# Kernel tuning notes

Hardware: AMD Instinct MI355X
Metric: run time of the kernel (lower is better)

The kernel has to match this reference:

```python
import jax, jax.numpy as jnp
import numpy as np

N_MOD = 2      # len(l_matrix)
N_SUB = 4096   # each l_matrix entry
DIM = 64
K = 20
ALPHA = 3.0
N = N_MOD * N_SUB  # 8192 total nodes


def setup_inputs() -> dict:
    key = jax.random.key(0)
    k1, k2, k3, k4 = jax.random.split(key, 4)
    nmat = N_MOD * N_MOD
    emb1 = 0.1 * jax.random.normal(k1, (nmat, N_SUB, DIM), dtype=jnp.float32)
    emb2 = 0.1 * jax.random.normal(k2, (nmat, N_SUB, DIM), dtype=jnp.float32)
    # __init__ sets w1/w2 to identity, b to zeros; perturb slightly so they matter
    eye = jnp.eye(DIM, dtype=jnp.float32)
    w1 = eye[None] + 0.01 * jax.random.normal(k3, (nmat, DIM, DIM), dtype=jnp.float32)
    w2 = eye[None] + 0.01 * jax.random.normal(k4, (nmat, DIM, DIM), dtype=jnp.float32)
    b1 = jnp.zeros((nmat, DIM), dtype=jnp.float32)
    b2 = jnp.zeros((nmat, DIM), dtype=jnp.float32)
    idx = jnp.arange(N, dtype=jnp.int64) if jax.config.jax_enable_x64 else jnp.arange(N, dtype=jnp.int32)
    return {"idx": idx, "emb1": emb1, "emb2": emb2, "w1": w1, "w2": w2, "b1": b1, "b2": b2}


def reference(idx, emb1, emb2, w1, w2, b1, b2):
    # per-block linear: nodevec = emb @ w + b   (batched over the nmatrix blocks)
    v1 = jnp.einsum('knd,kde->kne', emb1, w1) + b1[:, None, :]   # [nmat, N_SUB, DIM]
    v2 = jnp.einsum('kmd,kde->kme', emb2, w2) + b2[:, None, :]
    # per-block score: relu(tanh(alpha * v1 @ v2^T))
    a = jnp.einsum('kne,kme->knm', v1, v2)                       # [nmat, N_SUB, N_SUB]
    blocks = jax.nn.relu(jnp.tanh(ALPHA * a))
    # assemble full adjacency: block (i,j) at index i*n_mod + j
    adj = blocks.reshape(N_MOD, N_MOD, N_SUB, N_SUB)
    adj = adj.transpose(0, 2, 1, 3).reshape(N, N)                # [N, N]
    # row-wise topk mask (mask=1 at topk positions), adj * mask
    vals, cols = jax.lax.top_k(adj, K)                           # [N, K]
    rows = jnp.arange(N)[:, None]
    out = jnp.zeros_like(adj).at[rows, cols].set(vals)
    return out


if __name__ == "__main__":
    out = reference(**setup_inputs())
    print(out.shape, float(out.sum()))
```

## Files before the change

### kernel.cpp

```cpp
#include <hip/hip_runtime.h>
#include <hip/hip_bf16.h>

#define NSUB 4096
#define DIM 64
#define NROW 8192
#define KTOP 20
#define CAND 64

typedef unsigned long long u64;
typedef __attribute__((ext_vector_type(8))) short bf16x8;
typedef __attribute__((ext_vector_type(4))) float f32x4;

__device__ __forceinline__ unsigned umax(unsigned a, unsigned b) { return a > b ? a : b; }
__device__ __forceinline__ unsigned umin(unsigned a, unsigned b) { return a < b ? a : b; }

__global__ __launch_bounds__(256) void k_compute_v(
        const float* __restrict__ emb1, const float* __restrict__ w1,
        const float* __restrict__ b1,
        const float* __restrict__ emb2, const float* __restrict__ w2,
        const float* __restrict__ b2,
        double* __restrict__ V1d, double* __restrict__ V2d,
        unsigned short* __restrict__ V1b, unsigned short* __restrict__ V2b) {
    __shared__ alignas(16) float embS[64 * 64];
    __shared__ alignas(16) float wS[64 * 64];
    __shared__ float bS[64];

    int bx    = blockIdx.x;
    int which = bx >> 8;
    int rem   = bx & 255;
    int k     = rem >> 6;
    int tile  = rem & 63;
    int n0    = tile * 64;

    const float* emb = which ? emb2 : emb1;
    const float* w   = which ? w2 : w1;
    const float* b   = which ? b2 : b1;
    double* Vd = which ? V2d : V1d;
    unsigned short* Vb = which ? V2b : V1b;

    int tid = threadIdx.x;
    const float* esrc = emb + ((size_t)k * NSUB + n0) * DIM;
    const float* wsrc = w + (size_t)k * DIM * DIM;
    for (int t = tid; t < 64 * 64; t += 256) { embS[t] = esrc[t]; wS[t] = wsrc[t]; }
    if (tid < 64) bS[tid] = b[k * 64 + tid];
    __syncthreads();

    int e    = tid & 63;
    int mrow = tid >> 6;

    double accs[16];
#pragma unroll
    for (int it = 0; it < 16; ++it) accs[it] = (double)bS[e];

    for (int dg = 0; dg < 16; ++dg) {
        double wv[4];
#pragma unroll
        for (int q = 0; q < 4; ++q) wv[q] = (double)wS[(dg * 4 + q) * 64 + e];
#pragma unroll
        for (int it = 0; it < 16; ++it) {
            float4 em = *(const float4*)&embS[(mrow * 16 + it) * 64 + dg * 4];
            accs[it] += (double)em.x * wv[0] + (double)em.y * wv[1]
                      + (double)em.z * wv[2] + (double)em.w * wv[3];
        }
    }

#pragma unroll
    for (int it = 0; it < 16; ++it) {
        size_t o = ((size_t)k * NSUB + n0 + mrow * 16 + it) * DIM + e;
        Vd[o] = accs[it];
        __hip_bfloat16 hv = __float2bfloat16((float)accs[it]);
        Vb[o] = *reinterpret_cast<unsigned short*>(&hv);
    }
}

__global__ __launch_bounds__(256) void k_stage1(const unsigned short* __restrict__ V1b,
                                                const unsigned short* __restrict__ V2b,
                                                unsigned int* __restrict__ S1) {
    int tid = threadIdx.x;
    int l = tid & 63;
    int w = tid >> 6;
    int bx = blockIdx.x;
    int r0 = (bx >> 1) * 64;
    int h  = bx & 1;
    int i  = r0 >> 12;
    int n0 = r0 & (NSUB - 1);
    int kb = 2 * i + h;
    int q  = l >> 4;

    bf16x8 a0[4], a1[4];
#pragma unroll
    for (int t = 0; t < 4; ++t) {
        const unsigned short* ap =
            V1b + ((size_t)kb * NSUB + n0 + t * 16 + (l & 15)) * DIM + (q * 8);
        a0[t] = *(const bf16x8*)ap;
        a1[t] = *(const bf16x8*)(ap + 32);
    }

    const unsigned short* bp =
        V2b + ((size_t)kb * NSUB + w * 1024 + (l & 15)) * DIM + (q * 8);

    float m1[16], m2[16];
#pragma unroll
    for (int sl = 0; sl < 16; ++sl) { m1[sl] = 0.f; m2[sl] = 0.f; }

    for (int s = 0; s < 64; ++s) {
        bf16x8 b0 = *(const bf16x8*)bp;
        bf16x8 b1v = *(const bf16x8*)(bp + 32);
        bp += 16 * DIM;
#pragma unroll
        for (int t = 0; t < 4; ++t) {
            f32x4 acc = {0.f, 0.f, 0.f, 0.f};
            acc = __builtin_amdgcn_mfma_f32_16x16x32_bf16(a0[t], b0, acc, 0, 0, 0);
            acc = __builtin_amdgcn_mfma_f32_16x16x32_bf16(a1[t], b1v, acc, 0, 0, 0);
#pragma unroll
            for (int r = 0; r < 4; ++r) {
                int sl = t * 4 + r;
                float v = acc[r];
                m2[sl] = __builtin_amdgcn_fmed3f(v, m1[sl], m2[sl]);
                m1[sl] = fmaxf(m1[sl], v);
            }
        }
        if ((s & 15) == 15) {
#pragma unroll
            for (int st = 1; st <= 8; st <<= 1) {
#pragma unroll
                for (int sl = 0; sl < 16; ++sl) {
                    float o1 = __shfl_xor(m1[sl], st);
                    float o2 = __shfl_xor(m2[sl], st);
                    float nm1 = fmaxf(m1[sl], o1);
                    float nm2 = fmaxf(fminf(m1[sl], o1), fmaxf(m2[sl], o2));
                    m1[sl] = nm1; m2[sl] = nm2;
                }
            }
            if ((l & 15) == 0) {
                int gblk = h * 16 + w * 4 + (s >> 4);
#pragma unroll
                for (int sl = 0; sl < 16; ++sl) {
                    int rowg = r0 + (sl >> 2) * 16 + q * 4 + (sl & 3);
                    uint2 vv;
                    vv.x = __float_as_uint(m1[sl]);
                    vv.y = __float_as_uint(m2[sl]);
                    *(uint2*)&S1[(size_t)rowg * 64 + gblk * 2] = vv;
                }
            }
#pragma unroll
            for (int sl = 0; sl < 16; ++sl) { m1[sl] = 0.f; m2[sl] = 0.f; }
        }
    }
}

__global__ __launch_bounds__(256) void k_thresh(const unsigned int* __restrict__ S1,
                                                float* __restrict__ Lth) {
    int tid = threadIdx.x;
    int l = tid & 63, w = tid >> 6;
    int row = blockIdx.x * 4 + w;
    unsigned key = S1[(size_t)row * 64 + l];
#pragma unroll
    for (int k = 2; k <= 64; k <<= 1) {
#pragma unroll
        for (int j = k >> 1; j > 0; j >>= 1) {
            unsigned other = (unsigned)__shfl_xor((int)key, j);
            int ixj = l ^ j;
            bool up = ((l & k) == 0);
            bool keepMax = ((l > ixj) == up);
            key = keepMax ? umax(key, other) : umin(key, other);
        }
    }
    if (l == 44) Lth[row] = fmaxf(__uint_as_float(key) - 0.006f, 1e-30f);
}

__global__ __launch_bounds__(256) void k_filter(const unsigned short* __restrict__ V1b,
                                                const unsigned short* __restrict__ V2b,
                                                const float* __restrict__ Lth,
                                                unsigned int* __restrict__ cnt,
                                                int* __restrict__ colsG) {
    __shared__ float Lsh[64];
    int tid = threadIdx.x;
    int l = tid & 63;
    int w = tid >> 6;
    int bx = blockIdx.x;
    int r0 = (bx >> 1) * 64;
    int h  = bx & 1;
    int i  = r0 >> 12;
    int n0 = r0 & (NSUB - 1);
    int kb = 2 * i + h;
    int q  = l >> 4;

    if (tid < 64) Lsh[tid] = Lth[r0 + tid];
    __syncthreads();

    bf16x8 a0[4], a1[4];
#pragma unroll
    for (int t = 0; t < 4; ++t) {
        const unsigned short* ap =
            V1b + ((size_t)kb * NSUB + n0 + t * 16 + (l & 15)) * DIM + (q * 8);
        a0[t] = *(const bf16x8*)ap;
        a1[t] = *(const bf16x8*)(ap + 32);
    }

    float Lr[16];
#pragma unroll
    for (int sl = 0; sl < 16; ++sl)
        Lr[sl] = Lsh[(sl >> 2) * 16 + q * 4 + (sl & 3)];

    const unsigned short* bp =
        V2b + ((size_t)kb * NSUB + w * 1024 + (l & 15)) * DIM + (q * 8);

    for (int s = 0; s < 64; ++s) {
        bf16x8 b0 = *(const bf16x8*)bp;
        bf16x8 b1v = *(const bf16x8*)(bp + 32);
        bp += 16 * DIM;
        int c = h * 4096 + w * 1024 + s * 16 + (l & 15);
#pragma unroll
        for (int t = 0; t < 4; ++t) {
            f32x4 acc = {0.f, 0.f, 0.f, 0.f};
            acc = __builtin_amdgcn_mfma_f32_16x16x32_bf16(a0[t], b0, acc, 0, 0, 0);
            acc = __builtin_amdgcn_mfma_f32_16x16x32_bf16(a1[t], b1v, acc, 0, 0, 0);
#pragma unroll
            for (int r = 0; r < 4; ++r) {
                int sl = t * 4 + r;
                if (acc[r] >= Lr[sl]) {
                    int rowg = r0 + t * 16 + q * 4 + r;
                    unsigned pos = atomicAdd(&cnt[rowg], 1u);
                    if (pos < CAND) colsG[(size_t)rowg * CAND + pos] = c;
                }
            }
        }
    }
}

__global__ __launch_bounds__(256) void k_refine(const double* __restrict__ V1d,
                                                const double* __restrict__ V2d,
                                                const unsigned int* __restrict__ cnt,
                                                const int* __restrict__ colsG,
                                                int* __restrict__ outIdx,
                                                float* __restrict__ outVal) {
    int tid = threadIdx.x;
    int l = tid & 63, w = tid >> 6;
    int row = blockIdx.x * 4 + w;
    int i = row >> 12, n = row & (NSUB - 1);

    unsigned cn = cnt[row];
    if (cn > CAND) cn = CAND;
    bool valid = (unsigned)l < cn;
    int c = valid ? colsG[(size_t)row * CAND + l] : 0;
    int k = 2 * i + (c >> 12);
    int m = c & (NSUB - 1);

    const double* v1p = V1d + ((size_t)k * NSUB + n) * DIM;
    const double* v2p = V2d + ((size_t)k * NSUB + m) * DIM;
    double a = 0.0;
    for (int d = 0; d < DIM; ++d) a += v1p[d] * v2p[d];

    double av = a > 0.0 ? a : 0.0;
    u64 key = (((u64)__double_as_longlong(av)) & ~0x1FFFull) | (u64)(8191 - c);
    if (!valid) key = 0;

    int rank = 0;
    for (int jj = 0; jj < 64; ++jj) {
        u64 kj = (u64)__shfl((long long)key, jj);
        rank += (kj > key || (kj == key && jj < l)) ? 1 : 0;
    }
    if (valid && rank < KTOP) {
        float val = (av > 0.0) ? (float)tanh(3.0 * av) : 0.0f;
        outIdx[(size_t)row * KTOP + rank] = c;
        outVal[(size_t)row * KTOP + rank] = val;
    }
}

__global__ __launch_bounds__(256) void k_write(const int* __restrict__ outIdx,
                                               const float* __restrict__ outVal,
                                               float* __restrict__ out) {
    int t = threadIdx.x;
    size_t base = (size_t)blockIdx.x * 4 * NROW;
    float4 z = {0.f, 0.f, 0.f, 0.f};
    float4* o4 = (float4*)(out + base);
#pragma unroll
    for (int it = 0; it < 32; ++it) o4[it * 256 + t] = z;
    __syncthreads();
    if (t < 4 * KTOP) {
        int row = blockIdx.x * 4 + t / KTOP;
        int c = outIdx[(size_t)blockIdx.x * 4 * KTOP + t];
        float v = outVal[(size_t)blockIdx.x * 4 * KTOP + t];
        out[(size_t)row * NROW + c] = v;
    }
}

extern "C" void kernel_launch(void* const* d_in, const int* in_sizes, int n_in,
                              void* d_out, int out_size, void* d_ws, size_t ws_size,
                              hipStream_t stream) {
    const float* emb1 = (const float*)d_in[1];
    const float* emb2 = (const float*)d_in[2];
    const float* w1   = (const float*)d_in[3];
    const float* w2   = (const float*)d_in[4];
    const float* b1   = (const float*)d_in[5];
    const float* b2   = (const float*)d_in[6];
    float* out = (float*)d_out;

    char* p = (char*)d_out;
    double*         V1d   = (double*)p;
    double*         V2d   = (double*)(p + (size_t)8 * 1024 * 1024);
    unsigned short* V1b   = (unsigned short*)(p + (size_t)16 * 1024 * 1024);
    unsigned short* V2b   = (unsigned short*)(p + (size_t)18 * 1024 * 1024);
    unsigned int*   S1    = (unsigned int*)(p + (size_t)20 * 1024 * 1024);
    int*            colsG = (int*)(p + (size_t)22 * 1024 * 1024);

    int*          outIdx = (int*)d_ws;
    float*        outVal = (float*)((char*)d_ws + (size_t)NROW * KTOP * sizeof(int));
    unsigned int* cntp   = (unsigned int*)((char*)d_ws + (size_t)2 * NROW * KTOP * sizeof(int));
    float*        Lth    = (float*)((char*)cntp + (size_t)NROW * sizeof(unsigned int));

    hipLaunchKernelGGL(k_compute_v, dim3(512), dim3(256), 0, stream,
                       emb1, w1, b1, emb2, w2, b2, V1d, V2d, V1b, V2b);
    hipMemsetAsync(cntp, 0, (size_t)NROW * sizeof(unsigned int), stream);
    hipLaunchKernelGGL(k_stage1, dim3(256), dim3(256), 0, stream, V1b, V2b, S1);
    hipLaunchKernelGGL(k_thresh, dim3(2048), dim3(256), 0, stream, S1, Lth);
    hipLaunchKernelGGL(k_filter, dim3(256), dim3(256), 0, stream, V1b, V2b, Lth, cntp, colsG);
    hipLaunchKernelGGL(k_refine, dim3(2048), dim3(256), 0, stream,
                       V1d, V2d, cntp, colsG, outIdx, outVal);
    hipLaunchKernelGGL(k_write, dim3(2048), dim3(256), 0, stream,
                       outIdx, outVal, out);
}
```

Baseline: 526.2 us.

## Split stage1/filter column range across twice the blocks, prefetch B, fuse threshold

Stage1 and filter now each launch 512 blocks, each covering half the column range, instead of 256 blocks. This fills more compute units on a GPU with 256 CUs. The B-operand loads are software-prefetched one iteration ahead. The threshold bitonic sort is folded into the filter kernel, which drops one launch and the Lth round trip through global memory. In exchange, each filter block now sorts all 64 of its rows redundantly, and the two column-half blocks duplicate that work.

```diff
diff --git a/kernel.cpp b/kernel.cpp
--- a/kernel.cpp
+++ b/kernel.cpp
@@ -80,8 +80,10 @@
     int l = tid & 63;
     int w = tid >> 6;
     int bx = blockIdx.x;
-    int r0 = (bx >> 1) * 64;
-    int h  = bx & 1;
+    int rt = bx >> 2;
+    int h  = (bx >> 1) & 1;
+    int q2 = bx & 1;
+    int r0 = rt * 64;
     int i  = r0 >> 12;
     int n0 = r0 & (NSUB - 1);
     int kb = 2 * i + h;
@@ -96,22 +98,30 @@
         a1[t] = *(const bf16x8*)(ap + 32);
     }
 
+    int coff = q2 * 2048 + w * 512;
     const unsigned short* bp =
-        V2b + ((size_t)kb * NSUB + w * 1024 + (l & 15)) * DIM + (q * 8);
+        V2b + ((size_t)kb * NSUB + coff + (l & 15)) * DIM + (q * 8);
 
     float m1[16], m2[16];
 #pragma unroll
     for (int sl = 0; sl < 16; ++sl) { m1[sl] = 0.f; m2[sl] = 0.f; }
 
-    for (int s = 0; s < 64; ++s) {
-        bf16x8 b0 = *(const bf16x8*)bp;
-        bf16x8 b1v = *(const bf16x8*)(bp + 32);
-        bp += 16 * DIM;
+    bf16x8 cb0 = *(const bf16x8*)bp;
+    bf16x8 cb1 = *(const bf16x8*)(bp + 32);
+    bp += 16 * DIM;
+
+    for (int s = 0; s < 32; ++s) {
+        bf16x8 nb0, nb1;
+        if (s < 31) {
+            nb0 = *(const bf16x8*)bp;
+            nb1 = *(const bf16x8*)(bp + 32);
+            bp += 16 * DIM;
+        }
 #pragma unroll
         for (int t = 0; t < 4; ++t) {
             f32x4 acc = {0.f, 0.f, 0.f, 0.f};
-            acc = __builtin_amdgcn_mfma_f32_16x16x32_bf16(a0[t], b0, acc, 0, 0, 0);
-            acc = __builtin_amdgcn_mfma_f32_16x16x32_bf16(a1[t], b1v, acc, 0, 0, 0);
+            acc = __builtin_amdgcn_mfma_f32_16x16x32_bf16(a0[t], cb0, acc, 0, 0, 0);
+            acc = __builtin_amdgcn_mfma_f32_16x16x32_bf16(a1[t], cb1, acc, 0, 0, 0);
 #pragma unroll
             for (int r = 0; r < 4; ++r) {
                 int sl = t * 4 + r;
@@ -133,7 +143,7 @@
                 }
             }
             if ((l & 15) == 0) {
-                int gblk = h * 16 + w * 4 + (s >> 4);
+                int gblk = h * 16 + q2 * 8 + w * 2 + (s >> 4);
 #pragma unroll
                 for (int sl = 0; sl < 16; ++sl) {
                     int rowg = r0 + (sl >> 2) * 16 + q * 4 + (sl & 3);
@@ -146,32 +156,13 @@
 #pragma unroll
             for (int sl = 0; sl < 16; ++sl) { m1[sl] = 0.f; m2[sl] = 0.f; }
         }
-    }
-}
-
-__global__ __launch_bounds__(256) void k_thresh(const unsigned int* __restrict__ S1,
-                                                float* __restrict__ Lth) {
-    int tid = threadIdx.x;
-    int l = tid & 63, w = tid >> 6;
-    int row = blockIdx.x * 4 + w;
-    unsigned key = S1[(size_t)row * 64 + l];
-#pragma unroll
-    for (int k = 2; k <= 64; k <<= 1) {
-#pragma unroll
-        for (int j = k >> 1; j > 0; j >>= 1) {
-            unsigned other = (unsigned)__shfl_xor((int)key, j);
-            int ixj = l ^ j;
-            bool up = ((l & k) == 0);
-            bool keepMax = ((l > ixj) == up);
-            key = keepMax ? umax(key, other) : umin(key, other);
-        }
-    }
-    if (l == 44) Lth[row] = fmaxf(__uint_as_float(key) - 0.006f, 1e-30f);
+        cb0 = nb0; cb1 = nb1;
+    }
 }
 
 __global__ __launch_bounds__(256) void k_filter(const unsigned short* __restrict__ V1b,
                                                 const unsigned short* __restrict__ V2b,
-                                                const float* __restrict__ Lth,
+                                                const unsigned int* __restrict__ S1,
                                                 unsigned int* __restrict__ cnt,
                                                 int* __restrict__ colsG) {
     __shared__ float Lsh[64];
@@ -179,14 +170,31 @@
     int l = tid & 63;
     int w = tid >> 6;
     int bx = blockIdx.x;
-    int r0 = (bx >> 1) * 64;
-    int h  = bx & 1;
+    int rt = bx >> 2;
+    int h  = (bx >> 1) & 1;
+    int q2 = bx & 1;
+    int r0 = rt * 64;
     int i  = r0 >> 12;
     int n0 = r0 & (NSUB - 1);
     int kb = 2 * i + h;
     int q  = l >> 4;
 
-    if (tid < 64) Lsh[tid] = Lth[r0 + tid];
+    for (int rr = 0; rr < 16; ++rr) {
+        int rowg = r0 + w * 16 + rr;
+        unsigned key = S1[(size_t)rowg * 64 + l];
+#pragma unroll
+        for (int k = 2; k <= 64; k <<= 1) {
+#pragma unroll
+            for (int j = k >> 1; j > 0; j >>= 1) {
+                unsigned other = (unsigned)__shfl_xor((int)key, j);
+                int ixj = l ^ j;
+                bool up = ((l & k) == 0);
+                bool keepMax = ((l > ixj) == up);
+                key = keepMax ? umax(key, other) : umin(key, other);
+            }
+        }
+        if (l == 44) Lsh[w * 16 + rr] = fmaxf(__uint_as_float(key) - 0.006f, 1e-30f);
+    }
     __syncthreads();
 
     bf16x8 a0[4], a1[4];
@@ -203,19 +211,27 @@
     for (int sl = 0; sl < 16; ++sl)
         Lr[sl] = Lsh[(sl >> 2) * 16 + q * 4 + (sl & 3)];
 
+    int coff = q2 * 2048 + w * 512;
     const unsigned short* bp =
-        V2b + ((size_t)kb * NSUB + w * 1024 + (l & 15)) * DIM + (q * 8);
-
-    for (int s = 0; s < 64; ++s) {
-        bf16x8 b0 = *(const bf16x8*)bp;
-        bf16x8 b1v = *(const bf16x8*)(bp + 32);
-        bp += 16 * DIM;
-        int c = h * 4096 + w * 1024 + s * 16 + (l & 15);
+        V2b + ((size_t)kb * NSUB + coff + (l & 15)) * DIM + (q * 8);
+
+    bf16x8 cb0 = *(const bf16x8*)bp;
+    bf16x8 cb1 = *(const bf16x8*)(bp + 32);
+    bp += 16 * DIM;
+
+    for (int s = 0; s < 32; ++s) {
+        bf16x8 nb0, nb1;
+        if (s < 31) {
+            nb0 = *(const bf16x8*)bp;
+            nb1 = *(const bf16x8*)(bp + 32);
+            bp += 16 * DIM;
+        }
+        int c = h * 4096 + coff + s * 16 + (l & 15);
 #pragma unroll
         for (int t = 0; t < 4; ++t) {
             f32x4 acc = {0.f, 0.f, 0.f, 0.f};
-            acc = __builtin_amdgcn_mfma_f32_16x16x32_bf16(a0[t], b0, acc, 0, 0, 0);
-            acc = __builtin_amdgcn_mfma_f32_16x16x32_bf16(a1[t], b1v, acc, 0, 0, 0);
+            acc = __builtin_amdgcn_mfma_f32_16x16x32_bf16(a0[t], cb0, acc, 0, 0, 0);
+            acc = __builtin_amdgcn_mfma_f32_16x16x32_bf16(a1[t], cb1, acc, 0, 0, 0);
 #pragma unroll
             for (int r = 0; r < 4; ++r) {
                 int sl = t * 4 + r;
@@ -226,6 +242,7 @@
                 }
             }
         }
+        cb0 = nb0; cb1 = nb1;
     }
 }
 
@@ -308,14 +325,12 @@
     int*          outIdx = (int*)d_ws;
     float*        outVal = (float*)((char*)d_ws + (size_t)NROW * KTOP * sizeof(int));
     unsigned int* cntp   = (unsigned int*)((char*)d_ws + (size_t)2 * NROW * KTOP * sizeof(int));
-    float*        Lth    = (float*)((char*)cntp + (size_t)NROW * sizeof(unsigned int));
 
     hipLaunchKernelGGL(k_compute_v, dim3(512), dim3(256), 0, stream,
                        emb1, w1, b1, emb2, w2, b2, V1d, V2d, V1b, V2b);
     hipMemsetAsync(cntp, 0, (size_t)NROW * sizeof(unsigned int), stream);
-    hipLaunchKernelGGL(k_stage1, dim3(256), dim3(256), 0, stream, V1b, V2b, S1);
-    hipLaunchKernelGGL(k_thresh, dim3(2048), dim3(256), 0, stream, S1, Lth);
-    hipLaunchKernelGGL(k_filter, dim3(256), dim3(256), 0, stream, V1b, V2b, Lth, cntp, colsG);
+    hipLaunchKernelGGL(k_stage1, dim3(512), dim3(256), 0, stream, V1b, V2b, S1);
+    hipLaunchKernelGGL(k_filter, dim3(512), dim3(256), 0, stream, V1b, V2b, S1, cntp, colsG);
     hipLaunchKernelGGL(k_refine, dim3(2048), dim3(256), 0, stream,
                        V1d, V2d, cntp, colsG, outIdx, outVal);
     hipLaunchKernelGGL(k_write, dim3(2048), dim3(256), 0, stream,
```

After: 448.7 us. 14.7% less time.
